# Performance work log

Hardware: AMD Instinct MI355X
Metric: run time of the kernel (lower is better)

The kernel has to match this reference:

```python
import jax, jax.numpy as jnp
import numpy as np

D_K = 128
SCALE = 1.0 / np.sqrt(D_K).astype(np.float32)


def setup_inputs() -> dict:
    key = jax.random.key(0)
    kq, kk, kv = jax.random.split(key, 3)
    B, S, D = 8, 2048, D_K
    Q = jax.random.normal(kq, (B, S, D), dtype=jnp.float32)
    K = jax.random.normal(kk, (B, S, D), dtype=jnp.float32)
    V = jax.random.normal(kv, (B, S, D), dtype=jnp.float32)
    # causal mask: 1 = attend, 0 = block (per docstring semantics)
    mask = jnp.tril(jnp.ones((S, S), dtype=jnp.int32))
    return {"Q": Q, "K": K, "V": V, "mask": mask}


def reference(Q, K, V, mask):
    # scores: (B, S, S)
    scores = jnp.einsum("bqd,bkd->bqk", Q, K) * SCALE
    scores = jnp.where(mask == 0, -jnp.inf, scores)
    attention_weights = jax.nn.softmax(scores, axis=-1)
    output = jnp.einsum("bqk,bkd->bqd", attention_weights, V)
    return (output, attention_weights)
```

## Files before the change

### kernel.cpp

```cpp
#include <hip/hip_runtime.h>
#include <stdint.h>

#define BATCH 8
#define SEQ 2048
#define DH 128
#define QT 32
#define KT 64

static constexpr float SCALE_F = 0.08838834764831843f;

using bf16x8 = __attribute__((ext_vector_type(8))) short;
using f32x4  = __attribute__((ext_vector_type(4))) float;

__device__ inline unsigned short f2bf(float f) {
  unsigned u = __float_as_uint(f);
  u += 0x7fff + ((u >> 16) & 1);
  return (unsigned short)(u >> 16);
}

extern "C" __global__ void __launch_bounds__(256)
convert_qk(const float4* __restrict__ Q, const float4* __restrict__ K,
           ushort4* __restrict__ Qb, ushort4* __restrict__ Kb) {
  int i = blockIdx.x * 256 + threadIdx.x;
  float4 q = Q[i];
  float4 k = K[i];
  ushort4 uq, uk;
  uq.x = f2bf(q.x); uq.y = f2bf(q.y); uq.z = f2bf(q.z); uq.w = f2bf(q.w);
  uk.x = f2bf(k.x); uk.y = f2bf(k.y); uk.z = f2bf(k.z); uk.w = f2bf(k.w);
  Qb[i] = uq;
  Kb[i] = uk;
}

extern "C" __global__ void __launch_bounds__(256)
convert_v(const float* __restrict__ V, unsigned short* __restrict__ Vt) {
  __shared__ __align__(16) unsigned short L[DH][72];
  const int b = blockIdx.x >> 5;
  const int st = blockIdx.x & 31;
  const int s0 = st * 64;
  const int tid = threadIdx.x;
  const float* Vb = V + ((size_t)b * SEQ + s0) * DH;
#pragma unroll
  for (int it = 0; it < 8; ++it) {
    int f = (it * 256 + tid) * 4;
    int r = f >> 7, d0 = f & 127;
    float4 v = *(const float4*)(Vb + f);
    L[d0 + 0][r] = f2bf(v.x);
    L[d0 + 1][r] = f2bf(v.y);
    L[d0 + 2][r] = f2bf(v.z);
    L[d0 + 3][r] = f2bf(v.w);
  }
  __syncthreads();
  const int d = tid >> 1, h = tid & 1;
  unsigned short* dst = Vt + ((size_t)b * DH + d) * SEQ + s0 + h * 32;
  const uint4* src = (const uint4*)&L[d][h * 32];
#pragma unroll
  for (int j = 0; j < 4; ++j) ((uint4*)dst)[j] = src[j];
}

__global__ __launch_bounds__(256, 2) void attn_one(
    const unsigned short* __restrict__ Qbf, const unsigned short* __restrict__ Kbf,
    const unsigned short* __restrict__ Vtg,
    float* __restrict__ Og, float* __restrict__ Wg) {
  __shared__ __align__(16) unsigned short Qs[QT][136];
  __shared__ __align__(16) unsigned short Ks[KT][136];
  __shared__ __align__(16) unsigned short Vs[DH][72];
  __shared__ __align__(16) unsigned short Ps[QT][72];
  __shared__ float red[4][QT];

  const int tid = threadIdx.x;
  const int lane = tid & 63;
  const int w = tid >> 6;
  const int l15 = lane & 15;
  const int quad = lane >> 4;

  const int b = blockIdx.x & 7;
  const int t = 63 - (blockIdx.x >> 3);
  const int q0 = t * QT;
  const int ntk = t / 2 + 1;

  const unsigned short* Qbb = Qbf + (size_t)b * SEQ * DH;
  const unsigned short* Kbb = Kbf + (size_t)b * SEQ * DH;
  const unsigned short* Vtb = Vtg + (size_t)b * DH * SEQ;
  float* Ob = Og + (size_t)b * SEQ * DH;
  float* Wb = Wg + (size_t)b * SEQ * SEQ;

  auto stageK = [&](int k0) {
#pragma unroll
    for (int it = 0; it < 4; ++it) {
      int f = (it * 256 + tid) * 8;
      int r = f >> 7, d0 = f & 127;
      *(uint4*)&Ks[r][d0] = *(const uint4*)(Kbb + (size_t)(k0 + r) * DH + d0);
    }
  };
  auto stageV = [&](int k0) {
#pragma unroll
    for (int it = 0; it < 4; ++it) {
      int f = (it * 256 + tid) * 8;
      int d = f >> 6, s0 = f & 63;
      *(uint4*)&Vs[d][s0] = *(const uint4*)(Vtb + (size_t)d * SEQ + k0 + s0);
    }
  };

  {
    const int c0f = ntk * KT;
    const int len = SEQ - c0f;
    if (len > 0) {
      const float4 z4 = {0.f, 0.f, 0.f, 0.f};
      for (int r = 0; r < QT; ++r) {
        float* row = Wb + (size_t)(q0 + r) * SEQ + c0f;
        for (int c = tid * 4; c < len; c += 1024) *(float4*)(row + c) = z4;
      }
    }
  }

#pragma unroll
  for (int it = 0; it < 2; ++it) {
    int f = (it * 256 + tid) * 8;
    int r = f >> 7, d0 = f & 127;
    *(uint4*)&Qs[r][d0] = *(const uint4*)(Qbb + (size_t)(q0 + r) * DH + d0);
  }

  float rs0[4] = {0.f, 0.f, 0.f, 0.f};
  float rs1[4] = {0.f, 0.f, 0.f, 0.f};
  for (int kt = 0; kt < ntk; ++kt) {
    __syncthreads();
    stageK(kt * KT);
    __syncthreads();
    f32x4 a0 = {0.f, 0.f, 0.f, 0.f};
    f32x4 a1 = {0.f, 0.f, 0.f, 0.f};
#pragma unroll
    for (int ks = 0; ks < 4; ++ks) {
      bf16x8 qa0 = *(const bf16x8*)&Qs[l15][ks * 32 + quad * 8];
      bf16x8 qa1 = *(const bf16x8*)&Qs[16 + l15][ks * 32 + quad * 8];
      bf16x8 kb = *(const bf16x8*)&Ks[w * 16 + l15][ks * 32 + quad * 8];
      a0 = __builtin_amdgcn_mfma_f32_16x16x32_bf16(qa0, kb, a0, 0, 0, 0);
      a1 = __builtin_amdgcn_mfma_f32_16x16x32_bf16(qa1, kb, a1, 0, 0, 0);
    }
    const int kcol = kt * KT + w * 16 + l15;
#pragma unroll
    for (int r = 0; r < 4; ++r) {
      const int row0 = q0 + quad * 4 + r;
      const int row1 = row0 + 16;
      rs0[r] += (kcol <= row0) ? __expf(a0[r] * SCALE_F) : 0.f;
      rs1[r] += (kcol <= row1) ? __expf(a1[r] * SCALE_F) : 0.f;
    }
  }
#pragma unroll
  for (int m = 1; m <= 8; m <<= 1) {
#pragma unroll
    for (int r = 0; r < 4; ++r) {
      rs0[r] += __shfl_xor(rs0[r], m);
      rs1[r] += __shfl_xor(rs1[r], m);
    }
  }
  __syncthreads();
  if (l15 == 0) {
#pragma unroll
    for (int r = 0; r < 4; ++r) {
      red[w][quad * 4 + r] = rs0[r];
      red[w][16 + quad * 4 + r] = rs1[r];
    }
  }
  __syncthreads();
  float inv0[4], inv1[4];
#pragma unroll
  for (int r = 0; r < 4; ++r) {
    float s0 = red[0][quad * 4 + r] + red[1][quad * 4 + r] +
               red[2][quad * 4 + r] + red[3][quad * 4 + r];
    float s1 = red[0][16 + quad * 4 + r] + red[1][16 + quad * 4 + r] +
               red[2][16 + quad * 4 + r] + red[3][16 + quad * 4 + r];
    inv0[r] = 1.f / s0;
    inv1[r] = 1.f / s1;
  }

  f32x4 o00 = {0.f, 0.f, 0.f, 0.f}, o01 = {0.f, 0.f, 0.f, 0.f};
  f32x4 o10 = {0.f, 0.f, 0.f, 0.f}, o11 = {0.f, 0.f, 0.f, 0.f};
  for (int kt = 0; kt < ntk; ++kt) {
    __syncthreads();
    stageK(kt * KT);
    stageV(kt * KT);
    __syncthreads();
    f32x4 a0 = {0.f, 0.f, 0.f, 0.f};
    f32x4 a1 = {0.f, 0.f, 0.f, 0.f};
#pragma unroll
    for (int ks = 0; ks < 4; ++ks) {
      bf16x8 qa0 = *(const bf16x8*)&Qs[l15][ks * 32 + quad * 8];
      bf16x8 qa1 = *(const bf16x8*)&Qs[16 + l15][ks * 32 + quad * 8];
      bf16x8 kb = *(const bf16x8*)&Ks[w * 16 + l15][ks * 32 + quad * 8];
      a0 = __builtin_amdgcn_mfma_f32_16x16x32_bf16(qa0, kb, a0, 0, 0, 0);
      a1 = __builtin_amdgcn_mfma_f32_16x16x32_bf16(qa1, kb, a1, 0, 0, 0);
    }
    const int kcol = kt * KT + w * 16 + l15;
#pragma unroll
    for (int r = 0; r < 4; ++r) {
      const int row0 = q0 + quad * 4 + r;
      const int row1 = row0 + 16;
      float p0 = (kcol <= row0) ? __expf(a0[r] * SCALE_F) * inv0[r] : 0.f;
      float p1 = (kcol <= row1) ? __expf(a1[r] * SCALE_F) * inv1[r] : 0.f;
      Wb[(size_t)row0 * SEQ + kcol] = p0;
      Wb[(size_t)row1 * SEQ + kcol] = p1;
      Ps[quad * 4 + r][w * 16 + l15] = f2bf(p0);
      Ps[16 + quad * 4 + r][w * 16 + l15] = f2bf(p1);
    }
    __syncthreads();
#pragma unroll
    for (int ks = 0; ks < 2; ++ks) {
      bf16x8 pa0 = *(const bf16x8*)&Ps[l15][ks * 32 + quad * 8];
      bf16x8 pa1 = *(const bf16x8*)&Ps[16 + l15][ks * 32 + quad * 8];
      bf16x8 v0 = *(const bf16x8*)&Vs[w * 32 + l15][ks * 32 + quad * 8];
      bf16x8 v1 = *(const bf16x8*)&Vs[w * 32 + 16 + l15][ks * 32 + quad * 8];
      o00 = __builtin_amdgcn_mfma_f32_16x16x32_bf16(pa0, v0, o00, 0, 0, 0);
      o01 = __builtin_amdgcn_mfma_f32_16x16x32_bf16(pa0, v1, o01, 0, 0, 0);
      o10 = __builtin_amdgcn_mfma_f32_16x16x32_bf16(pa1, v0, o10, 0, 0, 0);
      o11 = __builtin_amdgcn_mfma_f32_16x16x32_bf16(pa1, v1, o11, 0, 0, 0);
    }
  }

#pragma unroll
  for (int r = 0; r < 4; ++r) {
    const int row0 = q0 + quad * 4 + r;
    const int row1 = row0 + 16;
    Ob[(size_t)row0 * DH + w * 32 + l15] = o00[r];
    Ob[(size_t)row0 * DH + w * 32 + 16 + l15] = o01[r];
    Ob[(size_t)row1 * DH + w * 32 + l15] = o10[r];
    Ob[(size_t)row1 * DH + w * 32 + 16 + l15] = o11[r];
  }
}

__global__ __launch_bounds__(256, 2) void attn_fb(
    const float* __restrict__ Qg, const float* __restrict__ Kg,
    const float* __restrict__ Vg, float* __restrict__ Og, float* __restrict__ Wg) {
  __shared__ __align__(16) unsigned short Qs[QT][136];
  __shared__ __align__(16) unsigned short Ks[KT][136];
  __shared__ __align__(16) unsigned short Vs[DH][72];
  __shared__ __align__(16) unsigned short Ps[QT][72];
  __shared__ float red[4][QT];

  const int tid = threadIdx.x;
  const int lane = tid & 63;
  const int w = tid >> 6;
  const int l15 = lane & 15;
  const int quad = lane >> 4;

  const int b = blockIdx.x >> 5;
  const int z = blockIdx.x & 31;

  const float* Qgb = Qg + (size_t)b * SEQ * DH;
  const float* Kgb = Kg + (size_t)b * SEQ * DH;
  const float* Vgb = Vg + (size_t)b * SEQ * DH;
  float* Ob = Og + (size_t)b * SEQ * DH;
  float* Wb = Wg + (size_t)b * SEQ * SEQ;

  auto stageK = [&](int k0) {
#pragma unroll
    for (int it = 0; it < 8; ++it) {
      int f = (it * 256 + tid) * 4;
      int r = f >> 7, d0 = f & 127;
      float4 v = *(const float4*)(Kgb + (size_t)(k0 + r) * DH + d0);
      ushort4 u;
      u.x = f2bf(v.x); u.y = f2bf(v.y); u.z = f2bf(v.z); u.w = f2bf(v.w);
      *(ushort4*)&Ks[r][d0] = u;
    }
  };
  auto stageV = [&](int k0) {
#pragma unroll
    for (int it = 0; it < 8; ++it) {
      int f = (it * 256 + tid) * 4;
      int r = f >> 7, d0 = f & 127;
      float4 v = *(const float4*)(Vgb + (size_t)(k0 + r) * DH + d0);
      Vs[d0 + 0][r] = f2bf(v.x);
      Vs[d0 + 1][r] = f2bf(v.y);
      Vs[d0 + 2][r] = f2bf(v.z);
      Vs[d0 + 3][r] = f2bf(v.w);
    }
  };

  const int tiles[2] = {z, 63 - z};
  for (int ti = 0; ti < 2; ++ti) {
    const int t = tiles[ti];
    const int q0 = t * QT;
    const int ntk = t / 2 + 1;
    {
      const int c0f = ntk * KT;
      const int len = SEQ - c0f;
      if (len > 0) {
        const float4 z4 = {0.f, 0.f, 0.f, 0.f};
        for (int r = 0; r < QT; ++r) {
          float* row = Wb + (size_t)(q0 + r) * SEQ + c0f;
          for (int c = tid * 4; c < len; c += 1024) *(float4*)(row + c) = z4;
        }
      }
    }
    __syncthreads();
#pragma unroll
    for (int it = 0; it < 4; ++it) {
      int f = (it * 256 + tid) * 4;
      int r = f >> 7, d0 = f & 127;
      float4 v = *(const float4*)(Qgb + (size_t)(q0 + r) * DH + d0);
      ushort4 u;
      u.x = f2bf(v.x); u.y = f2bf(v.y); u.z = f2bf(v.z); u.w = f2bf(v.w);
      *(ushort4*)&Qs[r][d0] = u;
    }
    float rs0[4] = {0.f, 0.f, 0.f, 0.f};
    float rs1[4] = {0.f, 0.f, 0.f, 0.f};
    for (int kt = 0; kt < ntk; ++kt) {
      __syncthreads();
      stageK(kt * KT);
      __syncthreads();
      f32x4 a0 = {0.f, 0.f, 0.f, 0.f};
      f32x4 a1 = {0.f, 0.f, 0.f, 0.f};
#pragma unroll
      for (int ks = 0; ks < 4; ++ks) {
        bf16x8 qa0 = *(const bf16x8*)&Qs[l15][ks * 32 + quad * 8];
        bf16x8 qa1 = *(const bf16x8*)&Qs[16 + l15][ks * 32 + quad * 8];
        bf16x8 kb = *(const bf16x8*)&Ks[w * 16 + l15][ks * 32 + quad * 8];
        a0 = __builtin_amdgcn_mfma_f32_16x16x32_bf16(qa0, kb, a0, 0, 0, 0);
        a1 = __builtin_amdgcn_mfma_f32_16x16x32_bf16(qa1, kb, a1, 0, 0, 0);
      }
      const int kcol = kt * KT + w * 16 + l15;
#pragma unroll
      for (int r = 0; r < 4; ++r) {
        const int row0 = q0 + quad * 4 + r;
        const int row1 = row0 + 16;
        rs0[r] += (kcol <= row0) ? __expf(a0[r] * SCALE_F) : 0.f;
        rs1[r] += (kcol <= row1) ? __expf(a1[r] * SCALE_F) : 0.f;
      }
    }
#pragma unroll
    for (int m = 1; m <= 8; m <<= 1) {
#pragma unroll
      for (int r = 0; r < 4; ++r) {
        rs0[r] += __shfl_xor(rs0[r], m);
        rs1[r] += __shfl_xor(rs1[r], m);
      }
    }
    __syncthreads();
    if (l15 == 0) {
#pragma unroll
      for (int r = 0; r < 4; ++r) {
        red[w][quad * 4 + r] = rs0[r];
        red[w][16 + quad * 4 + r] = rs1[r];
      }
    }
    __syncthreads();
    float inv0[4], inv1[4];
#pragma unroll
    for (int r = 0; r < 4; ++r) {
      float s0 = red[0][quad * 4 + r] + red[1][quad * 4 + r] +
                 red[2][quad * 4 + r] + red[3][quad * 4 + r];
      float s1 = red[0][16 + quad * 4 + r] + red[1][16 + quad * 4 + r] +
                 red[2][16 + quad * 4 + r] + red[3][16 + quad * 4 + r];
      inv0[r] = 1.f / s0;
      inv1[r] = 1.f / s1;
    }
    f32x4 o00 = {0.f, 0.f, 0.f, 0.f}, o01 = {0.f, 0.f, 0.f, 0.f};
    f32x4 o10 = {0.f, 0.f, 0.f, 0.f}, o11 = {0.f, 0.f, 0.f, 0.f};
    for (int kt = 0; kt < ntk; ++kt) {
      __syncthreads();
      stageK(kt * KT);
      stageV(kt * KT);
      __syncthreads();
      f32x4 a0 = {0.f, 0.f, 0.f, 0.f};
      f32x4 a1 = {0.f, 0.f, 0.f, 0.f};
#pragma unroll
      for (int ks = 0; ks < 4; ++ks) {
        bf16x8 qa0 = *(const bf16x8*)&Qs[l15][ks * 32 + quad * 8];
        bf16x8 qa1 = *(const bf16x8*)&Qs[16 + l15][ks * 32 + quad * 8];
        bf16x8 kb = *(const bf16x8*)&Ks[w * 16 + l15][ks * 32 + quad * 8];
        a0 = __builtin_amdgcn_mfma_f32_16x16x32_bf16(qa0, kb, a0, 0, 0, 0);
        a1 = __builtin_amdgcn_mfma_f32_16x16x32_bf16(qa1, kb, a1, 0, 0, 0);
      }
      const int kcol = kt * KT + w * 16 + l15;
#pragma unroll
      for (int r = 0; r < 4; ++r) {
        const int row0 = q0 + quad * 4 + r;
        const int row1 = row0 + 16;
        float p0 = (kcol <= row0) ? __expf(a0[r] * SCALE_F) * inv0[r] : 0.f;
        float p1 = (kcol <= row1) ? __expf(a1[r] * SCALE_F) * inv1[r] : 0.f;
        Wb[(size_t)row0 * SEQ + kcol] = p0;
        Wb[(size_t)row1 * SEQ + kcol] = p1;
        Ps[quad * 4 + r][w * 16 + l15] = f2bf(p0);
        Ps[16 + quad * 4 + r][w * 16 + l15] = f2bf(p1);
      }
      __syncthreads();
#pragma unroll
      for (int ks = 0; ks < 2; ++ks) {
        bf16x8 pa0 = *(const bf16x8*)&Ps[l15][ks * 32 + quad * 8];
        bf16x8 pa1 = *(const bf16x8*)&Ps[16 + l15][ks * 32 + quad * 8];
        bf16x8 v0 = *(const bf16x8*)&Vs[w * 32 + l15][ks * 32 + quad * 8];
        bf16x8 v1 = *(const bf16x8*)&Vs[w * 32 + 16 + l15][ks * 32 + quad * 8];
        o00 = __builtin_amdgcn_mfma_f32_16x16x32_bf16(pa0, v0, o00, 0, 0, 0);
        o01 = __builtin_amdgcn_mfma_f32_16x16x32_bf16(pa0, v1, o01, 0, 0, 0);
        o10 = __builtin_amdgcn_mfma_f32_16x16x32_bf16(pa1, v0, o10, 0, 0, 0);
        o11 = __builtin_amdgcn_mfma_f32_16x16x32_bf16(pa1, v1, o11, 0, 0, 0);
      }
    }
#pragma unroll
    for (int r = 0; r < 4; ++r) {
      const int row0 = q0 + quad * 4 + r;
      const int row1 = row0 + 16;
      Ob[(size_t)row0 * DH + w * 32 + l15] = o00[r];
      Ob[(size_t)row0 * DH + w * 32 + 16 + l15] = o01[r];
      Ob[(size_t)row1 * DH + w * 32 + l15] = o10[r];
      Ob[(size_t)row1 * DH + w * 32 + 16 + l15] = o11[r];
    }
  }
}

extern "C" void kernel_launch(void* const* d_in, const int* in_sizes, int n_in,
                              void* d_out, int out_size, void* d_ws, size_t ws_size,
                              hipStream_t stream) {
  const float* Q = (const float*)d_in[0];
  const float* K = (const float*)d_in[1];
  const float* V = (const float*)d_in[2];
  float* Out = (float*)d_out;
  float* W = Out + (size_t)BATCH * SEQ * DH;

  const size_t nel = (size_t)BATCH * SEQ * DH;
  const size_t need = nel * 2 * 3;
  if (ws_size >= need) {
    unsigned short* Qbf = (unsigned short*)d_ws;
    unsigned short* Kbf = Qbf + nel;
    unsigned short* Vt = Kbf + nel;
    hipLaunchKernelGGL(convert_qk, dim3((unsigned)(nel / 4 / 256)), dim3(256), 0, stream,
                       (const float4*)Q, (const float4*)K, (ushort4*)Qbf, (ushort4*)Kbf);
    hipLaunchKernelGGL(convert_v, dim3(BATCH * (SEQ / 64)), dim3(256), 0, stream, V, Vt);
    hipLaunchKernelGGL(attn_one, dim3(BATCH * 64), dim3(256), 0, stream,
                       Qbf, Kbf, Vt, Out, W);
  } else {
    hipLaunchKernelGGL(attn_fb, dim3(BATCH * 32), dim3(256), 0, stream,
                       Q, K, V, Out, W);
  }
}
```

Baseline: 222.4 us.

## Double-buffer K/V tiles with register prefetch and keep Q fragments in registers

```diff
diff --git a/kernel.cpp b/kernel.cpp
--- a/kernel.cpp
+++ b/kernel.cpp
@@ -61,9 +61,8 @@
     const unsigned short* __restrict__ Qbf, const unsigned short* __restrict__ Kbf,
     const unsigned short* __restrict__ Vtg,
     float* __restrict__ Og, float* __restrict__ Wg) {
-  __shared__ __align__(16) unsigned short Qs[QT][136];
-  __shared__ __align__(16) unsigned short Ks[KT][136];
-  __shared__ __align__(16) unsigned short Vs[DH][72];
+  __shared__ __align__(16) unsigned short Ks[2][KT][136];
+  __shared__ __align__(16) unsigned short Vs[2][DH][72];
   __shared__ __align__(16) unsigned short Ps[QT][72];
   __shared__ float red[4][QT];
 
@@ -83,23 +82,6 @@
   const unsigned short* Vtb = Vtg + (size_t)b * DH * SEQ;
   float* Ob = Og + (size_t)b * SEQ * DH;
   float* Wb = Wg + (size_t)b * SEQ * SEQ;
-
-  auto stageK = [&](int k0) {
-#pragma unroll
-    for (int it = 0; it < 4; ++it) {
-      int f = (it * 256 + tid) * 8;
-      int r = f >> 7, d0 = f & 127;
-      *(uint4*)&Ks[r][d0] = *(const uint4*)(Kbb + (size_t)(k0 + r) * DH + d0);
-    }
-  };
-  auto stageV = [&](int k0) {
-#pragma unroll
-    for (int it = 0; it < 4; ++it) {
-      int f = (it * 256 + tid) * 8;
-      int d = f >> 6, s0 = f & 63;
-      *(uint4*)&Vs[d][s0] = *(const uint4*)(Vtb + (size_t)d * SEQ + k0 + s0);
-    }
-  };
 
   {
     const int c0f = ntk * KT;
@@ -113,29 +95,46 @@
     }
   }
 
-#pragma unroll
-  for (int it = 0; it < 2; ++it) {
+  bf16x8 qf0[4], qf1[4];
+#pragma unroll
+  for (int ks = 0; ks < 4; ++ks) {
+    qf0[ks] = *(const bf16x8*)(Qbb + (size_t)(q0 + l15) * DH + ks * 32 + quad * 8);
+    qf1[ks] = *(const bf16x8*)(Qbb + (size_t)(q0 + 16 + l15) * DH + ks * 32 + quad * 8);
+  }
+
+#pragma unroll
+  for (int it = 0; it < 4; ++it) {
     int f = (it * 256 + tid) * 8;
     int r = f >> 7, d0 = f & 127;
-    *(uint4*)&Qs[r][d0] = *(const uint4*)(Qbb + (size_t)(q0 + r) * DH + d0);
-  }
+    *(uint4*)&Ks[0][r][d0] = *(const uint4*)(Kbb + (size_t)r * DH + d0);
+  }
+  __syncthreads();
 
   float rs0[4] = {0.f, 0.f, 0.f, 0.f};
   float rs1[4] = {0.f, 0.f, 0.f, 0.f};
+  int cur = 0;
   for (int kt = 0; kt < ntk; ++kt) {
-    __syncthreads();
-    stageK(kt * KT);
-    __syncthreads();
+    const bool nxt = (kt + 1) < ntk;
+    uint4 kst[4];
+    if (nxt) {
+      const int k0 = (kt + 1) * KT;
+#pragma unroll
+      for (int it = 0; it < 4; ++it) {
+        int f = (it * 256 + tid) * 8;
+        int r = f >> 7, d0 = f & 127;
+        kst[it] = *(const uint4*)(Kbb + (size_t)(k0 + r) * DH + d0);
+      }
+    }
     f32x4 a0 = {0.f, 0.f, 0.f, 0.f};
     f32x4 a1 = {0.f, 0.f, 0.f, 0.f};
+    __builtin_amdgcn_s_setprio(1);
 #pragma unroll
     for (int ks = 0; ks < 4; ++ks) {
-      bf16x8 qa0 = *(const bf16x8*)&Qs[l15][ks * 32 + quad * 8];
-      bf16x8 qa1 = *(const bf16x8*)&Qs[16 + l15][ks * 32 + quad * 8];
-      bf16x8 kb = *(const bf16x8*)&Ks[w * 16 + l15][ks * 32 + quad * 8];
-      a0 = __builtin_amdgcn_mfma_f32_16x16x32_bf16(qa0, kb, a0, 0, 0, 0);
-      a1 = __builtin_amdgcn_mfma_f32_16x16x32_bf16(qa1, kb, a1, 0, 0, 0);
-    }
+      bf16x8 kb = *(const bf16x8*)&Ks[cur][w * 16 + l15][ks * 32 + quad * 8];
+      a0 = __builtin_amdgcn_mfma_f32_16x16x32_bf16(qf0[ks], kb, a0, 0, 0, 0);
+      a1 = __builtin_amdgcn_mfma_f32_16x16x32_bf16(qf1[ks], kb, a1, 0, 0, 0);
+    }
+    __builtin_amdgcn_s_setprio(0);
     const int kcol = kt * KT + w * 16 + l15;
 #pragma unroll
     for (int r = 0; r < 4; ++r) {
@@ -144,7 +143,18 @@
       rs0[r] += (kcol <= row0) ? __expf(a0[r] * SCALE_F) : 0.f;
       rs1[r] += (kcol <= row1) ? __expf(a1[r] * SCALE_F) : 0.f;
     }
-  }
+    if (nxt) {
+#pragma unroll
+      for (int it = 0; it < 4; ++it) {
+        int f = (it * 256 + tid) * 8;
+        int r = f >> 7, d0 = f & 127;
+        *(uint4*)&Ks[cur ^ 1][r][d0] = kst[it];
+      }
+    }
+    __syncthreads();
+    cur ^= 1;
+  }
+
 #pragma unroll
   for (int m = 1; m <= 8; m <<= 1) {
 #pragma unroll
@@ -173,23 +183,51 @@
     inv1[r] = 1.f / s1;
   }
 
+#pragma unroll
+  for (int it = 0; it < 4; ++it) {
+    int f = (it * 256 + tid) * 8;
+    int r = f >> 7, d0 = f & 127;
+    *(uint4*)&Ks[0][r][d0] = *(const uint4*)(Kbb + (size_t)r * DH + d0);
+  }
+#pragma unroll
+  for (int it = 0; it < 4; ++it) {
+    int f = (it * 256 + tid) * 8;
+    int d = f >> 6, s0 = f & 63;
+    *(uint4*)&Vs[0][d][s0] = *(const uint4*)(Vtb + (size_t)d * SEQ + s0);
+  }
+  __syncthreads();
+
   f32x4 o00 = {0.f, 0.f, 0.f, 0.f}, o01 = {0.f, 0.f, 0.f, 0.f};
   f32x4 o10 = {0.f, 0.f, 0.f, 0.f}, o11 = {0.f, 0.f, 0.f, 0.f};
+  cur = 0;
   for (int kt = 0; kt < ntk; ++kt) {
-    __syncthreads();
-    stageK(kt * KT);
-    stageV(kt * KT);
-    __syncthreads();
+    const bool nxt = (kt + 1) < ntk;
+    uint4 kst[4], vst[4];
+    if (nxt) {
+      const int k0 = (kt + 1) * KT;
+#pragma unroll
+      for (int it = 0; it < 4; ++it) {
+        int f = (it * 256 + tid) * 8;
+        int r = f >> 7, d0 = f & 127;
+        kst[it] = *(const uint4*)(Kbb + (size_t)(k0 + r) * DH + d0);
+      }
+#pragma unroll
+      for (int it = 0; it < 4; ++it) {
+        int f = (it * 256 + tid) * 8;
+        int d = f >> 6, s0 = f & 63;
+        vst[it] = *(const uint4*)(Vtb + (size_t)d * SEQ + k0 + s0);
+      }
+    }
     f32x4 a0 = {0.f, 0.f, 0.f, 0.f};
     f32x4 a1 = {0.f, 0.f, 0.f, 0.f};
+    __builtin_amdgcn_s_setprio(1);
 #pragma unroll
     for (int ks = 0; ks < 4; ++ks) {
-      bf16x8 qa0 = *(const bf16x8*)&Qs[l15][ks * 32 + quad * 8];
-      bf16x8 qa1 = *(const bf16x8*)&Qs[16 + l15][ks * 32 + quad * 8];
-      bf16x8 kb = *(const bf16x8*)&Ks[w * 16 + l15][ks * 32 + quad * 8];
-      a0 = __builtin_amdgcn_mfma_f32_16x16x32_bf16(qa0, kb, a0, 0, 0, 0);
-      a1 = __builtin_amdgcn_mfma_f32_16x16x32_bf16(qa1, kb, a1, 0, 0, 0);
-    }
+      bf16x8 kb = *(const bf16x8*)&Ks[cur][w * 16 + l15][ks * 32 + quad * 8];
+      a0 = __builtin_amdgcn_mfma_f32_16x16x32_bf16(qf0[ks], kb, a0, 0, 0, 0);
+      a1 = __builtin_amdgcn_mfma_f32_16x16x32_bf16(qf1[ks], kb, a1, 0, 0, 0);
+    }
+    __builtin_amdgcn_s_setprio(0);
     const int kcol = kt * KT + w * 16 + l15;
 #pragma unroll
     for (int r = 0; r < 4; ++r) {
@@ -203,17 +241,35 @@
       Ps[16 + quad * 4 + r][w * 16 + l15] = f2bf(p1);
     }
     __syncthreads();
+    __builtin_amdgcn_s_setprio(1);
 #pragma unroll
     for (int ks = 0; ks < 2; ++ks) {
       bf16x8 pa0 = *(const bf16x8*)&Ps[l15][ks * 32 + quad * 8];
       bf16x8 pa1 = *(const bf16x8*)&Ps[16 + l15][ks * 32 + quad * 8];
-      bf16x8 v0 = *(const bf16x8*)&Vs[w * 32 + l15][ks * 32 + quad * 8];
-      bf16x8 v1 = *(const bf16x8*)&Vs[w * 32 + 16 + l15][ks * 32 + quad * 8];
+      bf16x8 v0 = *(const bf16x8*)&Vs[cur][w * 32 + l15][ks * 32 + quad * 8];
+      bf16x8 v1 = *(const bf16x8*)&Vs[cur][w * 32 + 16 + l15][ks * 32 + quad * 8];
       o00 = __builtin_amdgcn_mfma_f32_16x16x32_bf16(pa0, v0, o00, 0, 0, 0);
       o01 = __builtin_amdgcn_mfma_f32_16x16x32_bf16(pa0, v1, o01, 0, 0, 0);
       o10 = __builtin_amdgcn_mfma_f32_16x16x32_bf16(pa1, v0, o10, 0, 0, 0);
       o11 = __builtin_amdgcn_mfma_f32_16x16x32_bf16(pa1, v1, o11, 0, 0, 0);
     }
+    __builtin_amdgcn_s_setprio(0);
+    if (nxt) {
+#pragma unroll
+      for (int it = 0; it < 4; ++it) {
+        int f = (it * 256 + tid) * 8;
+        int r = f >> 7, d0 = f & 127;
+        *(uint4*)&Ks[cur ^ 1][r][d0] = kst[it];
+      }
+#pragma unroll
+      for (int it = 0; it < 4; ++it) {
+        int f = (it * 256 + tid) * 8;
+        int d = f >> 6, s0 = f & 63;
+        *(uint4*)&Vs[cur ^ 1][d][s0] = vst[it];
+      }
+    }
+    __syncthreads();
+    cur ^= 1;
   }
 
 #pragma unroll
```

Result: slower. 320.1 us (+43.9%).

## Double-buffer K/V tiles with direct global-to-LDS loads and swizzled layout

Applied to the files above, without the earlier changes.

```diff
diff --git a/kernel.cpp b/kernel.cpp
--- a/kernel.cpp
+++ b/kernel.cpp
@@ -16,6 +16,12 @@
   unsigned u = __float_as_uint(f);
   u += 0x7fff + ((u >> 16) & 1);
   return (unsigned short)(u >> 16);
+}
+
+__device__ inline void gload_lds16(const void* g, void* l) {
+  __builtin_amdgcn_global_load_lds(
+      (const __attribute__((address_space(1))) void*)g,
+      (__attribute__((address_space(3))) void*)l, 16, 0, 0);
 }
 
 extern "C" __global__ void __launch_bounds__(256)
@@ -28,7 +34,10 @@
   uq.x = f2bf(q.x); uq.y = f2bf(q.y); uq.z = f2bf(q.z); uq.w = f2bf(q.w);
   uk.x = f2bf(k.x); uk.y = f2bf(k.y); uk.z = f2bf(k.z); uk.w = f2bf(k.w);
   Qb[i] = uq;
-  Kb[i] = uk;
+  int r = i >> 5;
+  int byte = (i & 31) * 8;
+  int sbyte = byte ^ ((r & 7) << 4);
+  Kb[(size_t)r * 32 + (sbyte >> 3)] = uk;
 }
 
 extern "C" __global__ void __launch_bounds__(256)
@@ -51,10 +60,13 @@
   }
   __syncthreads();
   const int d = tid >> 1, h = tid & 1;
-  unsigned short* dst = Vt + ((size_t)b * DH + d) * SEQ + s0 + h * 32;
+  unsigned short* dstb = Vt + ((size_t)b * DH + d) * SEQ + s0;
   const uint4* src = (const uint4*)&L[d][h * 32];
 #pragma unroll
-  for (int j = 0; j < 4; ++j) ((uint4*)dst)[j] = src[j];
+  for (int j = 0; j < 4; ++j) {
+    int u = h * 4 + j;
+    ((uint4*)dstb)[u ^ (d & 7)] = src[j];
+  }
 }
 
 __global__ __launch_bounds__(256, 2) void attn_one(
@@ -62,8 +74,8 @@
     const unsigned short* __restrict__ Vtg,
     float* __restrict__ Og, float* __restrict__ Wg) {
   __shared__ __align__(16) unsigned short Qs[QT][136];
-  __shared__ __align__(16) unsigned short Ks[KT][136];
-  __shared__ __align__(16) unsigned short Vs[DH][72];
+  __shared__ __align__(16) unsigned short Ks[2][KT][128];
+  __shared__ __align__(16) unsigned short Vs[2][DH][64];
   __shared__ __align__(16) unsigned short Ps[QT][72];
   __shared__ float red[4][QT];
 
@@ -72,6 +84,7 @@
   const int w = tid >> 6;
   const int l15 = lane & 15;
   const int quad = lane >> 4;
+  const int swz = (l15 & 7) << 4;
 
   const int b = blockIdx.x & 7;
   const int t = 63 - (blockIdx.x >> 3);
@@ -84,20 +97,22 @@
   float* Ob = Og + (size_t)b * SEQ * DH;
   float* Wb = Wg + (size_t)b * SEQ * SEQ;
 
-  auto stageK = [&](int k0) {
+  auto stageK = [&](int buf, int k0) {
 #pragma unroll
     for (int it = 0; it < 4; ++it) {
-      int f = (it * 256 + tid) * 8;
-      int r = f >> 7, d0 = f & 127;
-      *(uint4*)&Ks[r][d0] = *(const uint4*)(Kbb + (size_t)(k0 + r) * DH + d0);
+      const unsigned short* g = Kbb + (size_t)k0 * DH + (it * 256 + tid) * 8;
+      unsigned short* l = &Ks[buf][0][0] + (it * 256 + w * 64) * 8;
+      gload_lds16(g, l);
     }
   };
-  auto stageV = [&](int k0) {
+  auto stageV = [&](int buf, int k0) {
 #pragma unroll
     for (int it = 0; it < 4; ++it) {
-      int f = (it * 256 + tid) * 8;
-      int d = f >> 6, s0 = f & 63;
-      *(uint4*)&Vs[d][s0] = *(const uint4*)(Vtb + (size_t)d * SEQ + k0 + s0);
+      int f = it * 256 + tid;
+      int d = f >> 3, u = f & 7;
+      const unsigned short* g = Vtb + (size_t)d * SEQ + k0 + u * 8;
+      unsigned short* l = &Vs[buf][0][0] + (it * 256 + w * 64) * 8;
+      gload_lds16(g, l);
     }
   };
 
@@ -119,20 +134,22 @@
     int r = f >> 7, d0 = f & 127;
     *(uint4*)&Qs[r][d0] = *(const uint4*)(Qbb + (size_t)(q0 + r) * DH + d0);
   }
+  stageK(0, 0);
+  __syncthreads();
 
   float rs0[4] = {0.f, 0.f, 0.f, 0.f};
   float rs1[4] = {0.f, 0.f, 0.f, 0.f};
+  int cur = 0;
   for (int kt = 0; kt < ntk; ++kt) {
-    __syncthreads();
-    stageK(kt * KT);
-    __syncthreads();
+    if (kt + 1 < ntk) stageK(cur ^ 1, (kt + 1) * KT);
     f32x4 a0 = {0.f, 0.f, 0.f, 0.f};
     f32x4 a1 = {0.f, 0.f, 0.f, 0.f};
 #pragma unroll
     for (int ks = 0; ks < 4; ++ks) {
       bf16x8 qa0 = *(const bf16x8*)&Qs[l15][ks * 32 + quad * 8];
       bf16x8 qa1 = *(const bf16x8*)&Qs[16 + l15][ks * 32 + quad * 8];
-      bf16x8 kb = *(const bf16x8*)&Ks[w * 16 + l15][ks * 32 + quad * 8];
+      const int cb = ((ks * 64 + quad * 16) ^ swz) >> 1;
+      bf16x8 kb = *(const bf16x8*)(&Ks[cur][0][0] + (w * 16 + l15) * 128 + cb);
       a0 = __builtin_amdgcn_mfma_f32_16x16x32_bf16(qa0, kb, a0, 0, 0, 0);
       a1 = __builtin_amdgcn_mfma_f32_16x16x32_bf16(qa1, kb, a1, 0, 0, 0);
     }
@@ -144,7 +161,13 @@
       rs0[r] += (kcol <= row0) ? __expf(a0[r] * SCALE_F) : 0.f;
       rs1[r] += (kcol <= row1) ? __expf(a1[r] * SCALE_F) : 0.f;
     }
-  }
+    __syncthreads();
+    cur ^= 1;
+  }
+
+  stageK(0, 0);
+  stageV(0, 0);
+
 #pragma unroll
   for (int m = 1; m <= 8; m <<= 1) {
 #pragma unroll
@@ -175,18 +198,20 @@
 
   f32x4 o00 = {0.f, 0.f, 0.f, 0.f}, o01 = {0.f, 0.f, 0.f, 0.f};
   f32x4 o10 = {0.f, 0.f, 0.f, 0.f}, o11 = {0.f, 0.f, 0.f, 0.f};
+  cur = 0;
   for (int kt = 0; kt < ntk; ++kt) {
-    __syncthreads();
-    stageK(kt * KT);
-    stageV(kt * KT);
-    __syncthreads();
+    if (kt + 1 < ntk) {
+      stageK(cur ^ 1, (kt + 1) * KT);
+      stageV(cur ^ 1, (kt + 1) * KT);
+    }
     f32x4 a0 = {0.f, 0.f, 0.f, 0.f};
     f32x4 a1 = {0.f, 0.f, 0.f, 0.f};
 #pragma unroll
     for (int ks = 0; ks < 4; ++ks) {
       bf16x8 qa0 = *(const bf16x8*)&Qs[l15][ks * 32 + quad * 8];
       bf16x8 qa1 = *(const bf16x8*)&Qs[16 + l15][ks * 32 + quad * 8];
-      bf16x8 kb = *(const bf16x8*)&Ks[w * 16 + l15][ks * 32 + quad * 8];
+      const int cb = ((ks * 64 + quad * 16) ^ swz) >> 1;
+      bf16x8 kb = *(const bf16x8*)(&Ks[cur][0][0] + (w * 16 + l15) * 128 + cb);
       a0 = __builtin_amdgcn_mfma_f32_16x16x32_bf16(qa0, kb, a0, 0, 0, 0);
       a1 = __builtin_amdgcn_mfma_f32_16x16x32_bf16(qa1, kb, a1, 0, 0, 0);
     }
@@ -207,13 +232,16 @@
     for (int ks = 0; ks < 2; ++ks) {
       bf16x8 pa0 = *(const bf16x8*)&Ps[l15][ks * 32 + quad * 8];
       bf16x8 pa1 = *(const bf16x8*)&Ps[16 + l15][ks * 32 + quad * 8];
-      bf16x8 v0 = *(const bf16x8*)&Vs[w * 32 + l15][ks * 32 + quad * 8];
-      bf16x8 v1 = *(const bf16x8*)&Vs[w * 32 + 16 + l15][ks * 32 + quad * 8];
+      const int cb = ((ks * 64 + quad * 16) ^ swz) >> 1;
+      bf16x8 v0 = *(const bf16x8*)(&Vs[cur][0][0] + (w * 32 + l15) * 64 + cb);
+      bf16x8 v1 = *(const bf16x8*)(&Vs[cur][0][0] + (w * 32 + 16 + l15) * 64 + cb);
       o00 = __builtin_amdgcn_mfma_f32_16x16x32_bf16(pa0, v0, o00, 0, 0, 0);
       o01 = __builtin_amdgcn_mfma_f32_16x16x32_bf16(pa0, v1, o01, 0, 0, 0);
       o10 = __builtin_amdgcn_mfma_f32_16x16x32_bf16(pa1, v0, o10, 0, 0, 0);
       o11 = __builtin_amdgcn_mfma_f32_16x16x32_bf16(pa1, v1, o11, 0, 0, 0);
     }
+    __syncthreads();
+    cur ^= 1;
   }
 
 #pragma unroll
```

After: 216.8 us. -2.6%, faster.

## Load Q/K/V fragments directly to registers and stage softmax weights for coalesced stores

Applied to the files above, without the earlier changes.

```diff
diff --git a/kernel.cpp b/kernel.cpp
--- a/kernel.cpp
+++ b/kernel.cpp
@@ -61,10 +61,8 @@
     const unsigned short* __restrict__ Qbf, const unsigned short* __restrict__ Kbf,
     const unsigned short* __restrict__ Vtg,
     float* __restrict__ Og, float* __restrict__ Wg) {
-  __shared__ __align__(16) unsigned short Qs[QT][136];
-  __shared__ __align__(16) unsigned short Ks[KT][136];
-  __shared__ __align__(16) unsigned short Vs[DH][72];
-  __shared__ __align__(16) unsigned short Ps[QT][72];
+  __shared__ __align__(16) unsigned short Ps[2][QT][72];
+  __shared__ __align__(16) float Psf[2][QT][68];
   __shared__ float red[4][QT];
 
   const int tid = threadIdx.x;
@@ -84,21 +82,20 @@
   float* Ob = Og + (size_t)b * SEQ * DH;
   float* Wb = Wg + (size_t)b * SEQ * SEQ;
 
-  auto stageK = [&](int k0) {
-#pragma unroll
-    for (int it = 0; it < 4; ++it) {
-      int f = (it * 256 + tid) * 8;
-      int r = f >> 7, d0 = f & 127;
-      *(uint4*)&Ks[r][d0] = *(const uint4*)(Kbb + (size_t)(k0 + r) * DH + d0);
-    }
+  const int rowK = w * 16 + l15;
+
+  auto loadK = [&](int k0, bf16x8* kf) {
+#pragma unroll
+    for (int ks = 0; ks < 4; ++ks)
+      kf[ks] = *(const bf16x8*)(Kbb + (size_t)(k0 + rowK) * DH + ks * 32 + quad * 8);
   };
-  auto stageV = [&](int k0) {
-#pragma unroll
-    for (int it = 0; it < 4; ++it) {
-      int f = (it * 256 + tid) * 8;
-      int d = f >> 6, s0 = f & 63;
-      *(uint4*)&Vs[d][s0] = *(const uint4*)(Vtb + (size_t)d * SEQ + k0 + s0);
-    }
+  auto loadV = [&](int k0, bf16x8* vf) {
+#pragma unroll
+    for (int ks = 0; ks < 2; ++ks)
+#pragma unroll
+      for (int j = 0; j < 2; ++j)
+        vf[ks * 2 + j] = *(const bf16x8*)(
+            Vtb + (size_t)(w * 32 + j * 16 + l15) * SEQ + k0 + ks * 32 + quad * 8);
   };
 
   {
@@ -113,38 +110,43 @@
     }
   }
 
-#pragma unroll
-  for (int it = 0; it < 2; ++it) {
-    int f = (it * 256 + tid) * 8;
-    int r = f >> 7, d0 = f & 127;
-    *(uint4*)&Qs[r][d0] = *(const uint4*)(Qbb + (size_t)(q0 + r) * DH + d0);
+  bf16x8 qf0[4], qf1[4];
+#pragma unroll
+  for (int ks = 0; ks < 4; ++ks) {
+    qf0[ks] = *(const bf16x8*)(Qbb + (size_t)(q0 + l15) * DH + ks * 32 + quad * 8);
+    qf1[ks] = *(const bf16x8*)(Qbb + (size_t)(q0 + 16 + l15) * DH + ks * 32 + quad * 8);
   }
 
   float rs0[4] = {0.f, 0.f, 0.f, 0.f};
   float rs1[4] = {0.f, 0.f, 0.f, 0.f};
-  for (int kt = 0; kt < ntk; ++kt) {
-    __syncthreads();
-    stageK(kt * KT);
-    __syncthreads();
-    f32x4 a0 = {0.f, 0.f, 0.f, 0.f};
-    f32x4 a1 = {0.f, 0.f, 0.f, 0.f};
-#pragma unroll
-    for (int ks = 0; ks < 4; ++ks) {
-      bf16x8 qa0 = *(const bf16x8*)&Qs[l15][ks * 32 + quad * 8];
-      bf16x8 qa1 = *(const bf16x8*)&Qs[16 + l15][ks * 32 + quad * 8];
-      bf16x8 kb = *(const bf16x8*)&Ks[w * 16 + l15][ks * 32 + quad * 8];
-      a0 = __builtin_amdgcn_mfma_f32_16x16x32_bf16(qa0, kb, a0, 0, 0, 0);
-      a1 = __builtin_amdgcn_mfma_f32_16x16x32_bf16(qa1, kb, a1, 0, 0, 0);
-    }
-    const int kcol = kt * KT + w * 16 + l15;
-#pragma unroll
-    for (int r = 0; r < 4; ++r) {
-      const int row0 = q0 + quad * 4 + r;
-      const int row1 = row0 + 16;
-      rs0[r] += (kcol <= row0) ? __expf(a0[r] * SCALE_F) : 0.f;
-      rs1[r] += (kcol <= row1) ? __expf(a1[r] * SCALE_F) : 0.f;
-    }
-  }
+  {
+    bf16x8 kc[4], kn[4];
+    loadK(0, kc);
+    for (int kt = 0; kt < ntk; ++kt) {
+      const bool nxt = (kt + 1) < ntk;
+      if (nxt) loadK((kt + 1) * KT, kn);
+      f32x4 a0 = {0.f, 0.f, 0.f, 0.f};
+      f32x4 a1 = {0.f, 0.f, 0.f, 0.f};
+#pragma unroll
+      for (int ks = 0; ks < 4; ++ks) {
+        a0 = __builtin_amdgcn_mfma_f32_16x16x32_bf16(qf0[ks], kc[ks], a0, 0, 0, 0);
+        a1 = __builtin_amdgcn_mfma_f32_16x16x32_bf16(qf1[ks], kc[ks], a1, 0, 0, 0);
+      }
+      const int kcol = kt * KT + rowK;
+#pragma unroll
+      for (int r = 0; r < 4; ++r) {
+        const int row0 = q0 + quad * 4 + r;
+        const int row1 = row0 + 16;
+        rs0[r] += (kcol <= row0) ? __expf(a0[r] * SCALE_F) : 0.f;
+        rs1[r] += (kcol <= row1) ? __expf(a1[r] * SCALE_F) : 0.f;
+      }
+      if (nxt) {
+#pragma unroll
+        for (int i = 0; i < 4; ++i) kc[i] = kn[i];
+      }
+    }
+  }
+
 #pragma unroll
   for (int m = 1; m <= 8; m <<= 1) {
 #pragma unroll
@@ -153,7 +155,6 @@
       rs1[r] += __shfl_xor(rs1[r], m);
     }
   }
-  __syncthreads();
   if (l15 == 0) {
 #pragma unroll
     for (int r = 0; r < 4; ++r) {
@@ -175,44 +176,56 @@
 
   f32x4 o00 = {0.f, 0.f, 0.f, 0.f}, o01 = {0.f, 0.f, 0.f, 0.f};
   f32x4 o10 = {0.f, 0.f, 0.f, 0.f}, o11 = {0.f, 0.f, 0.f, 0.f};
-  for (int kt = 0; kt < ntk; ++kt) {
-    __syncthreads();
-    stageK(kt * KT);
-    stageV(kt * KT);
-    __syncthreads();
-    f32x4 a0 = {0.f, 0.f, 0.f, 0.f};
-    f32x4 a1 = {0.f, 0.f, 0.f, 0.f};
-#pragma unroll
-    for (int ks = 0; ks < 4; ++ks) {
-      bf16x8 qa0 = *(const bf16x8*)&Qs[l15][ks * 32 + quad * 8];
-      bf16x8 qa1 = *(const bf16x8*)&Qs[16 + l15][ks * 32 + quad * 8];
-      bf16x8 kb = *(const bf16x8*)&Ks[w * 16 + l15][ks * 32 + quad * 8];
-      a0 = __builtin_amdgcn_mfma_f32_16x16x32_bf16(qa0, kb, a0, 0, 0, 0);
-      a1 = __builtin_amdgcn_mfma_f32_16x16x32_bf16(qa1, kb, a1, 0, 0, 0);
-    }
-    const int kcol = kt * KT + w * 16 + l15;
-#pragma unroll
-    for (int r = 0; r < 4; ++r) {
-      const int row0 = q0 + quad * 4 + r;
-      const int row1 = row0 + 16;
-      float p0 = (kcol <= row0) ? __expf(a0[r] * SCALE_F) * inv0[r] : 0.f;
-      float p1 = (kcol <= row1) ? __expf(a1[r] * SCALE_F) * inv1[r] : 0.f;
-      Wb[(size_t)row0 * SEQ + kcol] = p0;
-      Wb[(size_t)row1 * SEQ + kcol] = p1;
-      Ps[quad * 4 + r][w * 16 + l15] = f2bf(p0);
-      Ps[16 + quad * 4 + r][w * 16 + l15] = f2bf(p1);
-    }
-    __syncthreads();
-#pragma unroll
-    for (int ks = 0; ks < 2; ++ks) {
-      bf16x8 pa0 = *(const bf16x8*)&Ps[l15][ks * 32 + quad * 8];
-      bf16x8 pa1 = *(const bf16x8*)&Ps[16 + l15][ks * 32 + quad * 8];
-      bf16x8 v0 = *(const bf16x8*)&Vs[w * 32 + l15][ks * 32 + quad * 8];
-      bf16x8 v1 = *(const bf16x8*)&Vs[w * 32 + 16 + l15][ks * 32 + quad * 8];
-      o00 = __builtin_amdgcn_mfma_f32_16x16x32_bf16(pa0, v0, o00, 0, 0, 0);
-      o01 = __builtin_amdgcn_mfma_f32_16x16x32_bf16(pa0, v1, o01, 0, 0, 0);
-      o10 = __builtin_amdgcn_mfma_f32_16x16x32_bf16(pa1, v0, o10, 0, 0, 0);
-      o11 = __builtin_amdgcn_mfma_f32_16x16x32_bf16(pa1, v1, o11, 0, 0, 0);
+  {
+    bf16x8 kc[4], kn[4], vf[4];
+    loadK(0, kc);
+    const int srow = tid >> 3;
+    const int sc0 = (tid & 7) * 8;
+    for (int kt = 0; kt < ntk; ++kt) {
+      const int cur = kt & 1;
+      const bool nxt = (kt + 1) < ntk;
+      loadV(kt * KT, vf);
+      if (nxt) loadK((kt + 1) * KT, kn);
+      f32x4 a0 = {0.f, 0.f, 0.f, 0.f};
+      f32x4 a1 = {0.f, 0.f, 0.f, 0.f};
+#pragma unroll
+      for (int ks = 0; ks < 4; ++ks) {
+        a0 = __builtin_amdgcn_mfma_f32_16x16x32_bf16(qf0[ks], kc[ks], a0, 0, 0, 0);
+        a1 = __builtin_amdgcn_mfma_f32_16x16x32_bf16(qf1[ks], kc[ks], a1, 0, 0, 0);
+      }
+      const int kcol = kt * KT + rowK;
+#pragma unroll
+      for (int r = 0; r < 4; ++r) {
+        const int row0 = q0 + quad * 4 + r;
+        const int row1 = row0 + 16;
+        float p0 = (kcol <= row0) ? __expf(a0[r] * SCALE_F) * inv0[r] : 0.f;
+        float p1 = (kcol <= row1) ? __expf(a1[r] * SCALE_F) * inv1[r] : 0.f;
+        Ps[cur][quad * 4 + r][rowK] = f2bf(p0);
+        Ps[cur][16 + quad * 4 + r][rowK] = f2bf(p1);
+        Psf[cur][quad * 4 + r][rowK] = p0;
+        Psf[cur][16 + quad * 4 + r][rowK] = p1;
+      }
+      __syncthreads();
+#pragma unroll
+      for (int ks = 0; ks < 2; ++ks) {
+        bf16x8 pa0 = *(const bf16x8*)&Ps[cur][l15][ks * 32 + quad * 8];
+        bf16x8 pa1 = *(const bf16x8*)&Ps[cur][16 + l15][ks * 32 + quad * 8];
+        o00 = __builtin_amdgcn_mfma_f32_16x16x32_bf16(pa0, vf[ks * 2 + 0], o00, 0, 0, 0);
+        o01 = __builtin_amdgcn_mfma_f32_16x16x32_bf16(pa0, vf[ks * 2 + 1], o01, 0, 0, 0);
+        o10 = __builtin_amdgcn_mfma_f32_16x16x32_bf16(pa1, vf[ks * 2 + 0], o10, 0, 0, 0);
+        o11 = __builtin_amdgcn_mfma_f32_16x16x32_bf16(pa1, vf[ks * 2 + 1], o11, 0, 0, 0);
+      }
+      {
+        float4 x0 = *(const float4*)&Psf[cur][srow][sc0];
+        float4 x1 = *(const float4*)&Psf[cur][srow][sc0 + 4];
+        float* dst = Wb + (size_t)(q0 + srow) * SEQ + kt * KT + sc0;
+        *(float4*)dst = x0;
+        *(float4*)(dst + 4) = x1;
+      }
+      if (nxt) {
+#pragma unroll
+        for (int i = 0; i < 4; ++i) kc[i] = kn[i];
+      }
     }
   }
 
```

New measurement: 237.0 us. 6.5% more time.
